# Performance work log

Hardware: AMD Instinct MI355X
Metric: run time of the kernel (lower is better)

## Reference

```python
import jax, jax.numpy as jnp
import numpy as np

DIM = 32
B, H, W = 4, 256, 256


def conv1x1(x, w, b):
    # x: [B,C,H,W], w: [O,C], b: [O]
    return jnp.einsum('bchw,oc->bohw', x, w) + b[None, :, None, None]


def conv3x3(x, w, b):
    # x: [B,C,H,W], w: [O,C,3,3]
    out = jax.lax.conv_general_dilated(
        x, w, window_strides=(1, 1), padding='SAME',
        dimension_numbers=('NCHW', 'OIHW', 'NCHW'))
    return out + b[None, :, None, None]


def fft2d(x):
    # fft2 over last two dims, then fftshift over ALL dims (torch default)
    f = jnp.fft.fftshift(jnp.fft.fft2(x, norm='ortho'))
    return jnp.concatenate([f.real, f.imag], axis=1)  # [B,2C,H,W]


def ifft2d(x):
    f = jnp.fft.ifftshift(x)  # over ALL dims (torch default)
    re, im = jnp.split(f, 2, axis=1)
    c = jax.lax.complex(re, im)
    return jnp.abs(jnp.fft.ifft2(c, norm='ortho'))  # [B,C,H,W]


def setup_inputs() -> dict:
    key = jax.random.key(0)
    ks = jax.random.split(key, 16)
    C = DIM
    s = 0.02  # small init keeps the global-HW dot products in a sane softmax range
    inp = {
        'x': jax.random.normal(ks[0], (B, C, H, W), jnp.float32),
        'y': jax.random.normal(ks[1], (B, C, H, W), jnp.float32),
        'wq': jax.random.normal(ks[2], (C, C), jnp.float32) * s,
        'bq': jnp.zeros((C,), jnp.float32),
        'wk': jax.random.normal(ks[3], (C, C), jnp.float32) * s,
        'bk': jnp.zeros((C,), jnp.float32),
        'wv': jax.random.normal(ks[4], (C, C), jnp.float32) * s,
        'bv': jnp.zeros((C,), jnp.float32),
        'wd': jax.random.normal(ks[5], (C, C), jnp.float32) * s,
        'bd': jnp.zeros((C,), jnp.float32),
        'wc': jax.random.normal(ks[6], (2 * C, 2 * C, 3, 3), jnp.float32) * s,
        'bc': jnp.zeros((2 * C,), jnp.float32),
        'wi': jax.random.normal(ks[7], (2 * C, 2 * C, 3, 3), jnp.float32) * s,
        'bi': jnp.zeros((2 * C,), jnp.float32),
    }
    return inp


def reference(x, y, wq, bq, wk, bk, wv, bv, wd, bd, wc, bc, wi, bi):
    b, c, h, w = x.shape
    xq = conv1x1(x, wq, bq).reshape(b, c, h * w)            # [B,C,HW]
    dft = conv3x3(fft2d(conv1x1(y, wd, bd)), wc, bc)        # [B,2C,H,W]
    yk, yv = jnp.split(dft, 2, axis=1)
    yk = conv1x1(yk, wk, bk).reshape(b, c, h * w)
    yv = conv1x1(yv, wv, bv).reshape(b, c, h * w)
    att = jnp.einsum('bcn,bdn->bcd', xq, yk)                # [B,C,C]
    att = jax.nn.softmax(att, axis=1)                       # softmax over dim=1 (as in torch)
    out = jnp.einsum('bcd,bdn->bcn', att, yv).reshape(b, c, h, w)
    out = out + ifft2d(conv3x3(jax.nn.relu(dft), wi, bi))
    return out
```

## Files before the change

### kernel.cpp

```cpp
#include <hip/hip_runtime.h>
#include <math.h>

#define HW_ (256*256)
#define CH 32
#define CH2 64
#define BATCH 4

typedef short bf16x8 __attribute__((ext_vector_type(8)));
typedef float f32x4 __attribute__((ext_vector_type(4)));

__device__ __forceinline__ unsigned short f2bf(float f) {
    union { float f; unsigned u; } v; v.f = f;
    unsigned r = v.u + 0x7fffu + ((v.u >> 16) & 1u);
    return (unsigned short)(r >> 16);
}
__device__ __forceinline__ float bf2f(unsigned h) {
    union { unsigned u; float f; } v; v.u = h << 16;
    return v.f;
}

__device__ __forceinline__ int ctof_slot(int s) {
    return s < 16 ? s + 16 : s < 32 ? s + 32 : s < 48 ? s - 32 : s - 16;
}

__device__ __forceinline__ float2 cmul(float2 a, float2 b) {
    return make_float2(a.x*b.x - a.y*b.y, a.x*b.y + a.y*b.x);
}

__device__ __forceinline__ uint4 relu_bf16x8(uint4 v) {
    unsigned* pv = (unsigned*)&v;
    #pragma unroll
    for (int q = 0; q < 4; ++q) {
        unsigned a = pv[q];
        unsigned lo = a & 0xffffu, hi = a >> 16;
        if (lo & 0x8000u) lo = 0;
        if (hi & 0x8000u) hi = 0;
        pv[q] = lo | (hi << 16);
    }
    return v;
}

__device__ __forceinline__ void build_tw4(float2* tw, float sign) {
    int tid = threadIdx.x;
    float ang = sign * 6.2831853071795864769f * (float)tid / 256.0f;
    float s, c; sincosf(ang, &s, &c);
    tw[tid] = make_float2(c, s);
}

template<int SGN>
__device__ __forceinline__ void fft16_reg(float2* x, const float2* tw) {
    float2 u[16];
    #pragma unroll
    for (int m0 = 0; m0 < 4; ++m0) {
        float2 x0 = x[m0], x1 = x[m0+4], x2 = x[m0+8], x3 = x[m0+12];
        float2 t0 = make_float2(x0.x+x2.x, x0.y+x2.y);
        float2 t1 = make_float2(x0.x-x2.x, x0.y-x2.y);
        float2 t2 = make_float2(x1.x+x3.x, x1.y+x3.y);
        float2 t3 = make_float2(x1.x-x3.x, x1.y-x3.y);
        float2 r  = make_float2(-SGN*t3.y, SGN*t3.x);
        u[m0*4+0] = make_float2(t0.x+t2.x, t0.y+t2.y);
        u[m0*4+1] = make_float2(t1.x+r.x,  t1.y+r.y);
        u[m0*4+2] = make_float2(t0.x-t2.x, t0.y-t2.y);
        u[m0*4+3] = make_float2(t1.x-r.x,  t1.y-r.y);
    }
    #pragma unroll
    for (int m0 = 1; m0 < 4; ++m0)
        #pragma unroll
        for (int a = 1; a < 4; ++a)
            u[m0*4+a] = cmul(u[m0*4+a], tw[(16*m0*a) & 255]);
    #pragma unroll
    for (int a = 0; a < 4; ++a) {
        float2 x0 = u[a], x1 = u[4+a], x2 = u[8+a], x3 = u[12+a];
        float2 t0 = make_float2(x0.x+x2.x, x0.y+x2.y);
        float2 t1 = make_float2(x0.x-x2.x, x0.y-x2.y);
        float2 t2 = make_float2(x1.x+x3.x, x1.y+x3.y);
        float2 t3 = make_float2(x1.x-x3.x, x1.y-x3.y);
        float2 r  = make_float2(-SGN*t3.y, SGN*t3.x);
        x[a]    = make_float2(t0.x+t2.x, t0.y+t2.y);
        x[a+4]  = make_float2(t1.x+r.x,  t1.y+r.y);
        x[a+8]  = make_float2(t0.x-t2.x, t0.y-t2.y);
        x[a+12] = make_float2(t1.x-r.x,  t1.y-r.y);
    }
}

template<int SGN>
__device__ __forceinline__ void fft_core16(float2* A, const float2* tw) {
    const int tid = threadIdx.x;
    const int l = tid >> 4;
    const int d = tid & 15;
    const int base = l*257;
    float2 x[16];
    #pragma unroll
    for (int n1 = 0; n1 < 16; ++n1) x[n1] = A[base + n1*16 + d];
    fft16_reg<SGN>(x, tw);
    #pragma unroll
    for (int k0 = 1; k0 < 16; ++k0) x[k0] = cmul(x[k0], tw[d*k0]);
    #pragma unroll
    for (int k0 = 0; k0 < 16; ++k0) A[base + k0*16 + ((d + k0) & 15)] = x[k0];
    __syncthreads();
    #pragma unroll
    for (int n0 = 0; n0 < 16; ++n0) x[n0] = A[base + d*16 + ((n0 + d) & 15)];
    fft16_reg<SGN>(x, tw);
    #pragma unroll
    for (int k1 = 0; k1 < 16; ++k1) A[base + d + k1*16] = x[k1];
    __syncthreads();
}

__global__ __launch_bounds__(256) void k_fft_fwd1(const unsigned short* __restrict__ yd, ushort2* __restrict__ CAt) {
    __shared__ float2 A[16*257];
    __shared__ float2 tw[256];
    build_tw4(tw, -1.0f);
    int blk = blockIdx.x;
    int bp = blk >> 4, h0 = (blk & 15) << 4;
    int b = bp >> 4, p = bp & 15;
    const float sc = 1.0f/16.0f;
    const unsigned short* s0 = yd + ((size_t)(b*CH + 2*p))*HW_ + (size_t)h0*256;
    const unsigned short* s1 = s0 + HW_;
    for (int idx = threadIdx.x; idx < 16*64; idx += 256) {
        int l = idx >> 6, w4 = (idx & 63) << 2;
        uint2 va = *(const uint2*)(s0 + l*256 + w4);
        uint2 vb = *(const uint2*)(s1 + l*256 + w4);
        A[l*257 + w4+0] = make_float2(bf2f(va.x & 0xffffu)*sc, bf2f(vb.x & 0xffffu)*sc);
        A[l*257 + w4+1] = make_float2(bf2f(va.x >> 16)*sc, bf2f(vb.x >> 16)*sc);
        A[l*257 + w4+2] = make_float2(bf2f(va.y & 0xffffu)*sc, bf2f(vb.y & 0xffffu)*sc);
        A[l*257 + w4+3] = make_float2(bf2f(va.y >> 16)*sc, bf2f(vb.y >> 16)*sc);
    }
    __syncthreads();
    fft_core16<-1>(A, tw);
    int t = threadIdx.x;
    unsigned short pk[32];
    #pragma unroll
    for (int l = 0; l < 16; ++l) {
        float2 v = A[l*257 + t];
        pk[2*l]   = f2bf(v.x);
        pk[2*l+1] = f2bf(v.y);
    }
    uint4* d4 = (uint4*)(CAt + (size_t)bp*HW_ + (size_t)t*256 + h0);
    const uint4* s4 = (const uint4*)pk;
    d4[0] = s4[0]; d4[1] = s4[1]; d4[2] = s4[2]; d4[3] = s4[3];
}

__global__ __launch_bounds__(256) void k_fft_fwd2(const ushort2* __restrict__ CAt, unsigned short* __restrict__ FSH) {
    __shared__ float2 A[16*257];
    __shared__ float2 tw[256];
    build_tw4(tw, -1.0f);
    int blk = blockIdx.x;
    int b = blk >> 8, ph = (blk >> 7) & 1, vu = blk & 127;
    bool sp = (vu == 0);
    int col0 = vu, col1 = sp ? 128 : (256 - vu);
    const float sc = 1.0f/16.0f;
    for (int idx = threadIdx.x; idx < 16*256; idx += 256) {
        int l = idx >> 8, h = idx & 255;
        int p = l >> 1, s = l & 1;
        int col = s ? col1 : col0;
        ushort2 v = CAt[((size_t)(b*16 + ph*8 + p)*256 + col)*256 + h];
        A[l*257 + h] = make_float2(bf2f(v.x)*sc, bf2f(v.y)*sc);
    }
    __syncthreads();
    fft_core16<-1>(A, tw);
    int t = threadIdx.x;
    int bt = (b + 2) & 3;
    int ht = (t + 128) & 255;
    int tn = (256 - t) & 255;
    #pragma unroll
    for (int s = 0; s < 2; ++s) {
        int v = s ? col1 : col0;
        int wt = (v + 128) & 255;
        unsigned short pk[32];
        #pragma unroll
        for (int p = 0; p < 8; ++p) {
            int lA = 2*p + s;
            int lB = sp ? lA : (2*p + 1 - s);
            float2 Za = A[lA*257 + t];
            float2 Zb = A[lB*257 + tn];
            float xr = (Za.x + Zb.x)*0.5f, xi = (Za.y - Zb.y)*0.5f;
            float dr = Za.x - Zb.x,        di = Za.y + Zb.y;
            float yr = di*0.5f,            yi = -dr*0.5f;
            pk[2*p]     = f2bf(xr);
            pk[2*p+1]   = f2bf(yr);
            pk[16+2*p]  = f2bf(xi);
            pk[17+2*p]  = f2bf(yi);
        }
        unsigned short* dst = FSH + ((((size_t)bt*256 + ht)*256 + wt)*64 + ph*32);
        uint4* d4 = (uint4*)dst;
        const uint4* s4 = (const uint4*)pk;
        d4[0] = s4[0]; d4[1] = s4[1]; d4[2] = s4[2]; d4[3] = s4[3];
    }
}

__global__ __launch_bounds__(256) void k_conv1x1w(const float* __restrict__ in, const float* __restrict__ w,
                                                  const float* __restrict__ bias, unsigned short* __restrict__ out,
                                                  const float* __restrict__ wc, const float* __restrict__ wi,
                                                  unsigned short* __restrict__ d1, unsigned short* __restrict__ d2) {
    __shared__ float ts[32*257];
    int blk = blockIdx.x;
    int tid = threadIdx.x;
    if (blk >= 1024) {
        int i = (blk - 1024)*256 + tid;
        int half = i >= 36864;
        int j = i - half*36864;
        int tap = j >> 12, rem = j & 4095, oc = rem >> 6, s = rem & 63;
        if (half) {
            d2[j] = f2bf(wi[((size_t)(oc*64 + s))*9 + tap]);
        } else {
            int ic = ctof_slot(s);
            d1[j] = f2bf(wc[((size_t)(oc*64 + ic))*9 + tap]);
        }
        return;
    }
    int b = blk >> 8, h = blk & 255;
    const float* src = in + (size_t)b*CH*HW_ + (size_t)h*256;
    for (int idx = tid; idx < 32*256; idx += 256) {
        int c = idx >> 8, ww = idx & 255;
        ts[c*257 + ww] = src[(size_t)c*HW_ + ww];
    }
    __syncthreads();
    float acc[32];
    #pragma unroll
    for (int o = 0; o < 32; ++o) acc[o] = bias[o];
    for (int c = 0; c < 32; ++c) {
        float v = ts[c*257 + tid];
        #pragma unroll
        for (int o = 0; o < 32; ++o) acc[o] += w[o*32 + c] * v;
    }
    unsigned short* dst = out + (size_t)b*CH*HW_ + (size_t)h*256 + tid;
    #pragma unroll
    for (int o = 0; o < 32; ++o) dst[(size_t)o*HW_] = f2bf(acc[o]);
}

template<int MODE>
__global__ __launch_bounds__(256) void k_conv3(const unsigned short* __restrict__ in_cl,
                                               const unsigned short* __restrict__ wpk,
                                               const float* __restrict__ bias,
                                               unsigned short* __restrict__ outp) {
    __shared__ __align__(16) char Xs[2112*16];
    __shared__ __align__(16) char Ws[1536*16];
    int tid = threadIdx.x;
    int blk = blockIdx.x;
    int wseg = blk & 3, hg = (blk >> 2) & 63, b = blk >> 8;
    int h0 = hg*4, w0 = wseg*64;

    const uint4* wsrc = (const uint4*)wpk;

    for (int gl = tid; gl < 2112; gl += 256) {
        int slot = gl / 528;
        int rem  = gl - slot*528;
        int col  = rem >> 3, hseg = rem & 7;
        int hh = h0 - 1 + slot;
        int wcol = w0 - 1 + col;
        uint4 v = make_uint4(0,0,0,0);
        if (hh >= 0 && hh < 256 && wcol >= 0 && wcol < 256) {
            v = *(const uint4*)(in_cl + (((size_t)(b*256 + hh)*256 + wcol)*64) + hseg*8);
            if (MODE == 1) v = relu_bf16x8(v);
        }
        *(uint4*)(Xs + ((gl << 4) ^ ((col & 7) << 4))) = v;
    }
    #pragma unroll
    for (int q = 0; q < 6; ++q) {
        int gw = tid + q*256;
        int oc = (gw >> 3) & 63;
        *(uint4*)(Ws + ((gw << 4) ^ ((oc & 7) << 4))) = wsrc[gw];
    }
    __syncthreads();

    int lane = tid & 63;
    int wv = tid >> 6;
    int l16 = lane & 15, lq = lane >> 4;

    f32x4 acc[4][4];
    #pragma unroll
    for (int i = 0; i < 4; ++i)
        #pragma unroll
        for (int j = 0; j < 4; ++j) acc[i][j] = (f32x4)0.0f;

    for (int dy = 0; dy < 3; ++dy) {
        uint4 xr0 = make_uint4(0,0,0,0), xr1 = make_uint4(0,0,0,0), xr2 = make_uint4(0,0,0,0);
        uint4 wr[6];
        if (dy < 2) {
            int hh = h0 + dy + 3;
            bool hv = hh < 256;
            {
                int gl = tid;
                int col = gl >> 3, hseg = gl & 7;
                int wcol = w0 - 1 + col;
                if (hv && wcol >= 0 && wcol < 256)
                    xr0 = *(const uint4*)(in_cl + (((size_t)(b*256 + hh)*256 + wcol)*64) + hseg*8);
            }
            {
                int gl = tid + 256;
                int col = gl >> 3, hseg = gl & 7;
                int wcol = w0 - 1 + col;
                if (hv && wcol >= 0 && wcol < 256)
                    xr1 = *(const uint4*)(in_cl + (((size_t)(b*256 + hh)*256 + wcol)*64) + hseg*8);
            }
            if (tid < 16) {
                int gl = tid + 512;
                int col = gl >> 3, hseg = gl & 7;
                int wcol = w0 - 1 + col;
                if (hv && wcol < 256)
                    xr2 = *(const uint4*)(in_cl + (((size_t)(b*256 + hh)*256 + wcol)*64) + hseg*8);
            }
            #pragma unroll
            for (int q = 0; q < 6; ++q)
                wr[q] = wsrc[(dy+1)*1536 + tid + q*256];
        }

        int slot = (wv + dy) & 3;
        #pragma unroll
        for (int dx = 0; dx < 3; ++dx) {
            #pragma unroll
            for (int kk = 0; kk < 2; ++kk) {
                int hseg = kk*4 + lq;
                bf16x8 xf[4], wf[4];
                #pragma unroll
                for (int j = 0; j < 4; ++j) {
                    int col = j*16 + l16 + dx;
                    int g = slot*528 + col*8 + hseg;
                    xf[j] = *(const bf16x8*)(Xs + ((g << 4) ^ ((col & 7) << 4)));
                }
                #pragma unroll
                for (int i = 0; i < 4; ++i) {
                    int oc = i*16 + l16;
                    int lw = dx*512 + oc*8 + hseg;
                    wf[i] = *(const bf16x8*)(Ws + ((lw << 4) ^ ((oc & 7) << 4)));
                    #pragma unroll
                    for (int j = 0; j < 4; ++j) {
                        if (MODE == 0)
                            acc[i][j] = __builtin_amdgcn_mfma_f32_16x16x32_bf16(wf[i], xf[j], acc[i][j], 0, 0, 0);
                        else
                            acc[i][j] = __builtin_amdgcn_mfma_f32_16x16x32_bf16(xf[j], wf[i], acc[i][j], 0, 0, 0);
                    }
                }
            }
        }

        if (dy < 2) {
            __syncthreads();
            int slotn = dy & 3;
            {
                int gl = tid;
                int col = gl >> 3;
                uint4 v = (MODE == 1) ? relu_bf16x8(xr0) : xr0;
                int g = slotn*528 + gl;
                *(uint4*)(Xs + ((g << 4) ^ ((col & 7) << 4))) = v;
            }
            {
                int gl = tid + 256;
                int col = gl >> 3;
                uint4 v = (MODE == 1) ? relu_bf16x8(xr1) : xr1;
                int g = slotn*528 + gl;
                *(uint4*)(Xs + ((g << 4) ^ ((col & 7) << 4))) = v;
            }
            if (tid < 16) {
                int gl = tid + 512;
                int col = gl >> 3;
                uint4 v = (MODE == 1) ? relu_bf16x8(xr2) : xr2;
                int g = slotn*528 + gl;
                *(uint4*)(Xs + ((g << 4) ^ ((col & 7) << 4))) = v;
            }
            #pragma unroll
            for (int q = 0; q < 6; ++q) {
                int gw = tid + q*256;
                int oc = (gw >> 3) & 63;
                *(uint4*)(Ws + ((gw << 4) ^ ((oc & 7) << 4))) = wr[q];
            }
            __syncthreads();
        }
    }

    int h = h0 + wv;
    if (MODE == 0) {
        #pragma unroll
        for (int j = 0; j < 4; ++j) {
            int px = w0 + j*16 + l16;
            unsigned short* orow = outp + (((size_t)b*256 + h)*256 + px)*64;
            #pragma unroll
            for (int i = 0; i < 4; ++i) {
                int oc0 = i*16 + lq*4;
                float4 bv = *(const float4*)(bias + oc0);
                unsigned short c0 = f2bf(acc[i][j][0] + bv.x);
                unsigned short c1 = f2bf(acc[i][j][1] + bv.y);
                unsigned short c2 = f2bf(acc[i][j][2] + bv.z);
                unsigned short c3 = f2bf(acc[i][j][3] + bv.w);
                uint2 u;
                u.x = (unsigned)c0 | ((unsigned)c1 << 16);
                u.y = (unsigned)c2 | ((unsigned)c3 << 16);
                *(uint2*)(orow + oc0) = u;
            }
        }
    } else {
        #pragma unroll
        for (int i = 0; i < 4; ++i) {
            int oc = i*16 + l16;
            float bv = bias[oc];
            unsigned short* oplane = outp + ((size_t)b*64 + oc)*HW_ + (size_t)h*256;
            #pragma unroll
            for (int j = 0; j < 4; ++j) {
                int px0 = w0 + j*16 + lq*4;
                unsigned short c0 = f2bf(acc[i][j][0] + bv);
                unsigned short c1 = f2bf(acc[i][j][1] + bv);
                unsigned short c2 = f2bf(acc[i][j][2] + bv);
                unsigned short c3 = f2bf(acc[i][j][3] + bv);
                uint2 u;
                u.x = (unsigned)c0 | ((unsigned)c1 << 16);
                u.y = (unsigned)c2 | ((unsigned)c3 << 16);
                *(uint2*)(oplane + px0) = u;
            }
        }
    }
}

__global__ __launch_bounds__(256) void k_gram(const float* __restrict__ x, const unsigned short* __restrict__ dcl,
                                              float* __restrict__ Mpart, float* __restrict__ Sxp, float* __restrict__ Sdp) {
    __shared__ __align__(16) float xs[32*132];
    __shared__ __align__(16) unsigned short dst_[32*136];
    __shared__ float mred[1024];
    __shared__ float sxred[32];
    __shared__ float sdred[32];
    int blk = blockIdx.x;
    int b = blk >> 7, chunk = blk & 127;
    int tid = threadIdx.x, lane = tid & 63, wv = tid >> 6;
    int l16 = lane & 15, lq = lane >> 4;
    for (int idx = tid; idx < 1024; idx += 256) mred[idx] = 0.0f;
    if (tid < 32) { sxred[tid] = 0.0f; sdred[tid] = 0.0f; }

    const float* xb = x + (size_t)b*CH*HW_;
    const unsigned short* db = dcl + (size_t)b*HW_*64;

    f32x4 acc[2][2];
    #pragma unroll
    for (int i = 0; i < 2; ++i)
        #pragma unroll
        for (int j = 0; j < 2; ++j) acc[i][j] = (f32x4)0.0f;
    float sx0 = 0, sx1 = 0, sd0 = 0, sd1 = 0;

    for (int q4 = 0; q4 < 4; ++q4) {
        int px0 = chunk*512 + q4*128;
        __syncthreads();
        #pragma unroll
        for (int p = 0; p < 4; ++p) {
            int g = tid + p*256;
            int c = g >> 5, k4 = (g & 31) << 2;
            *(float4*)&xs[c*132 + k4] = *(const float4*)(xb + (size_t)c*HW_ + px0 + k4);
        }
        #pragma unroll
        for (int p = 0; p < 2; ++p) {
            int g = tid + p*256;
            int px = g >> 2, quad = g & 3;
            uint4 v = *(const uint4*)(db + (size_t)(px0 + px)*64 + quad*8);
            const unsigned short* pv = (const unsigned short*)&v;
            #pragma unroll
            for (int u = 0; u < 8; ++u) dst_[(quad*8 + u)*136 + px] = pv[u];
        }
        __syncthreads();
        #pragma unroll
        for (int ks = 0; ks < 4; ++ks) {
            int k0 = ks*32 + lq*8;
            float4 xa = *(const float4*)&xs[l16*132 + k0];
            float4 xc = *(const float4*)&xs[l16*132 + k0 + 4];
            float4 ya = *(const float4*)&xs[(16+l16)*132 + k0];
            float4 yc = *(const float4*)&xs[(16+l16)*132 + k0 + 4];
            bf16x8 a0, a1;
            const float* pxa = (const float*)&xa;
            const float* pxc = (const float*)&xc;
            const float* pya = (const float*)&ya;
            const float* pyc = (const float*)&yc;
            #pragma unroll
            for (int j = 0; j < 4; ++j) {
                a0[j]   = (short)f2bf(pxa[j]);  sx0 += pxa[j];
                a0[4+j] = (short)f2bf(pxc[j]);  sx0 += pxc[j];
                a1[j]   = (short)f2bf(pya[j]);  sx1 += pya[j];
                a1[4+j] = (short)f2bf(pyc[j]);  sx1 += pyc[j];
            }
            bf16x8 b0 = *(const bf16x8*)&dst_[l16*136 + k0];
            bf16x8 b1 = *(const bf16x8*)&dst_[(16+l16)*136 + k0];
            #pragma unroll
            for (int j = 0; j < 8; ++j) {
                sd0 += bf2f((unsigned short)b0[j]);
                sd1 += bf2f((unsigned short)b1[j]);
            }
            acc[0][0] = __builtin_amdgcn_mfma_f32_16x16x32_bf16(a0, b0, acc[0][0], 0, 0, 0);
            acc[0][1] = __builtin_amdgcn_mfma_f32_16x16x32_bf16(a0, b1, acc[0][1], 0, 0, 0);
            acc[1][0] = __builtin_amdgcn_mfma_f32_16x16x32_bf16(a1, b0, acc[1][0], 0, 0, 0);
            acc[1][1] = __builtin_amdgcn_mfma_f32_16x16x32_bf16(a1, b1, acc[1][1], 0, 0, 0);
        }
    }
    __syncthreads();

    #pragma unroll
    for (int fi = 0; fi < 2; ++fi)
        #pragma unroll
        for (int fj = 0; fj < 2; ++fj)
            #pragma unroll
            for (int r = 0; r < 4; ++r)
                atomicAdd(&mred[(fi*16 + lq*4 + r)*32 + fj*16 + l16], acc[fi][fj][r]);

    sx0 += __shfl_xor(sx0, 16); sx0 += __shfl_xor(sx0, 32);
    sx1 += __shfl_xor(sx1, 16); sx1 += __shfl_xor(sx1, 32);
    sd0 += __shfl_xor(sd0, 16); sd0 += __shfl_xor(sd0, 32);
    sd1 += __shfl_xor(sd1, 16); sd1 += __shfl_xor(sd1, 32);
    if (lane < 16) {
        atomicAdd(&sxred[l16], sx0);
        atomicAdd(&sxred[l16 + 16], sx1);
        atomicAdd(&sdred[l16], sd0);
        atomicAdd(&sdred[l16 + 16], sd1);
    }
    __syncthreads();

    float* mp = Mpart + ((size_t)(b*128 + chunk))*1024;
    for (int idx = tid; idx < 1024; idx += 256) mp[idx] = mred[idx];
    if (tid < 32) {
        Sxp[(b*128 + chunk)*32 + tid] = sxred[tid];
        Sdp[(b*128 + chunk)*32 + tid] = sdred[tid];
    }
}

__global__ __launch_bounds__(256) void k_att(const float* __restrict__ Mpart, const float* __restrict__ Sxp,
                                              const float* __restrict__ Sdp,
                                              const float* __restrict__ wq, const float* __restrict__ bq,
                                              const float* __restrict__ wk, const float* __restrict__ bk,
                                              const float* __restrict__ wv, const float* __restrict__ bv,
                                              float* __restrict__ att2, float* __restrict__ sout) {
    __shared__ float Mls[1024], T1[1024], attls[32*33];
    __shared__ float wqs[1024], wks[1024], wvs[1024];
    __shared__ float q1[32], k1[32], sxs[32], sds[32];
    int tid = threadIdx.x;
    int b = blockIdx.x;
    for (int idx = tid; idx < 1024; idx += 256) { wqs[idx] = wq[idx]; wks[idx] = wk[idx]; wvs[idx] = wv[idx]; }
    #pragma unroll
    for (int q = 0; q < 4; ++q) {
        int o = tid + q*256;
        float s = 0;
        for (int c = 0; c < 128; ++c) s += Mpart[((size_t)(b*128 + c))*1024 + o];
        Mls[o] = s;
    }
    if (tid < 32) { float s = 0; for (int c = 0; c < 128; ++c) s += Sxp[(b*128 + c)*32 + tid]; sxs[tid] = s; }
    else if (tid < 64) { int e = tid - 32; float s = 0; for (int c = 0; c < 128; ++c) s += Sdp[(b*128 + c)*32 + e]; sds[e] = s; }
    __syncthreads();
    if (tid < 32) { float s=0; for (int a=0;a<32;++a) s += wqs[tid*32+a]*sxs[a]; q1[tid]=s; }
    else if (tid < 64) { int d=tid-32; float s=0; for (int e=0;e<32;++e) s += wks[d*32+e]*sds[e]; k1[d]=s; }
    for (int idx = tid; idx < 1024; idx += 256) {
        int c = idx >> 5, e = idx & 31;
        float s = 0;
        for (int a=0;a<32;++a) s += wqs[c*32+a]*Mls[a*32+e];
        T1[idx] = s;
    }
    __syncthreads();
    for (int idx = tid; idx < 1024; idx += 256) {
        int c = idx >> 5, d = idx & 31;
        float s = 0;
        for (int e=0;e<32;++e) s += T1[c*32+e]*wks[d*32+e];
        s += bq[c]*k1[d] + bk[d]*q1[c] + 65536.0f*bq[c]*bk[d];
        attls[c*33+d] = s;
    }
    __syncthreads();
    if (tid < 32) {
        int d = tid;
        float mx = -1e30f;
        for (int c=0;c<32;++c) mx = fmaxf(mx, attls[c*33+d]);
        float sum = 0;
        for (int c=0;c<32;++c) { float e_ = expf(attls[c*33+d]-mx); attls[c*33+d]=e_; sum+=e_; }
        float inv = 1.0f/sum;
        for (int c=0;c<32;++c) attls[c*33+d] *= inv;
    }
    __syncthreads();
    for (int idx = tid; idx < 1024; idx += 256) {
        int c = idx >> 5, e = idx & 31;
        float s = 0;
        for (int d=0; d<32; ++d) s += attls[c*33+d]*wvs[d*32+e];
        att2[b*1024 + idx] = s;
    }
    if (tid < 32) {
        float s=0; for (int d=0;d<32;++d) s += attls[tid*33+d]*bv[d];
        sout[b*32+tid] = s;
    }
}

__global__ __launch_bounds__(256) void k_fft_inv1(const unsigned short* __restrict__ G, ushort2* __restrict__ Z1T) {
    __shared__ float2 A[16*257];
    __shared__ float2 tw[256];
    build_tw4(tw, 1.0f);
    int blk = blockIdx.x;
    int bc = blk >> 4, w0 = (blk & 15) << 4;
    int b = bc >> 5, c = bc & 31;
    int bs = (b + 2) & 3;
    const float sc = 1.0f/16.0f;
    const unsigned short* gre = G + ((size_t)(bs*CH2 + c + 32))*HW_;
    const unsigned short* gim = G + ((size_t)(bs*CH2 + c))*HW_;
    {
        int h = threadIdx.x;
        int hs = (h + 128) & 255;
        int wsb = (w0 + 128) & 255;
        const uint4* pr = (const uint4*)(gre + (size_t)hs*256 + wsb);
        const uint4* pi = (const uint4*)(gim + (size_t)hs*256 + wsb);
        uint4 r0 = pr[0], r1 = pr[1];
        uint4 i0 = pi[0], i1 = pi[1];
        unsigned short re[16], im[16];
        *(uint4*)&re[0] = r0; *(uint4*)&re[8] = r1;
        *(uint4*)&im[0] = i0; *(uint4*)&im[8] = i1;
        #pragma unroll
        for (int l = 0; l < 16; ++l)
            A[l*257 + h] = make_float2(bf2f(re[l])*sc, bf2f(im[l])*sc);
    }
    __syncthreads();
    fft_core16<1>(A, tw);
    ushort2* dst = Z1T + (size_t)bc*HW_;
    for (int idx = threadIdx.x; idx < 16*256; idx += 256) {
        int l = idx >> 8, h = idx & 255;
        float2 v = A[l*257 + h];
        dst[(size_t)(w0 + l)*256 + h] = make_ushort2(f2bf(v.x), f2bf(v.y));
    }
}

__global__ __launch_bounds__(256) void k_fft_inv2(const ushort2* __restrict__ Z1T, unsigned short* __restrict__ Mag) {
    __shared__ float2 A[16*257];
    __shared__ float2 tw[256];
    build_tw4(tw, 1.0f);
    int blk = blockIdx.x;
    int bc = blk >> 4, h0 = (blk & 15) << 4;
    const float sc = 1.0f/16.0f;
    {
        int w = threadIdx.x;
        const uint4* src = (const uint4*)(Z1T + (size_t)bc*HW_ + (size_t)w*256 + h0);
        uint4 t0 = src[0], t1 = src[1], t2 = src[2], t3 = src[3];
        ushort2 vv[16];
        *(uint4*)&vv[0]  = t0; *(uint4*)&vv[4]  = t1;
        *(uint4*)&vv[8]  = t2; *(uint4*)&vv[12] = t3;
        #pragma unroll
        for (int l = 0; l < 16; ++l)
            A[l*257 + w] = make_float2(bf2f(vv[l].x)*sc, bf2f(vv[l].y)*sc);
    }
    __syncthreads();
    fft_core16<1>(A, tw);
    unsigned short* dst = Mag + (size_t)bc*HW_ + (size_t)h0*256;
    for (int idx = threadIdx.x; idx < 16*256; idx += 256) {
        int l = idx >> 8, w = idx & 255;
        float2 v = A[l*257 + w];
        dst[l*256 + w] = f2bf(sqrtf(v.x*v.x + v.y*v.y));
    }
}

__global__ __launch_bounds__(256) void k_out(const unsigned short* __restrict__ dcl, const float* __restrict__ att2,
                                             const float* __restrict__ sv, const unsigned short* __restrict__ Mag,
                                             float* __restrict__ out) {
    __shared__ __align__(16) float A2ls[1024];
    __shared__ float svls[32];
    int blk = blockIdx.x; int b = blk >> 8, h = blk & 255;
    int tid = threadIdx.x;
    for (int idx = tid; idx < 1024; idx += 256) A2ls[idx] = att2[b*1024 + idx];
    if (tid < 32) svls[tid] = sv[b*32 + tid];
    __syncthreads();
    int px = tid;
    const uint4* dvp = (const uint4*)(dcl + ((((size_t)b*256 + h)*256 + px)*64 + 32));
    uint4 d0 = dvp[0], d1 = dvp[1];
    unsigned u[8] = {d0.x, d0.y, d0.z, d0.w, d1.x, d1.y, d1.z, d1.w};
    float dv[32];
    #pragma unroll
    for (int i = 0; i < 8; ++i) {
        dv[2*i]   = bf2f(u[i] & 0xffffu);
        dv[2*i+1] = bf2f(u[i] >> 16);
    }
    float accv[32];
    #pragma unroll
    for (int c = 0; c < 32; ++c) accv[c] = svls[c];
    #pragma unroll
    for (int q = 0; q < 8; ++q) {
        #pragma unroll
        for (int c = 0; c < 32; ++c) {
            float4 a4 = *(const float4*)&A2ls[c*32 + q*4];
            accv[c] += a4.x*dv[q*4] + a4.y*dv[q*4+1] + a4.z*dv[q*4+2] + a4.w*dv[q*4+3];
        }
    }
    const unsigned short* mb = Mag + (size_t)b*CH*HW_ + (size_t)h*256 + px;
    float* ob = out + (size_t)b*CH*HW_ + (size_t)h*256 + px;
    #pragma unroll
    for (int c = 0; c < 32; ++c) ob[(size_t)c*HW_] = accv[c] + bf2f(mb[(size_t)c*HW_]);
}

extern "C" void kernel_launch(void* const* d_in, const int* in_sizes, int n_in,
                              void* d_out, int out_size, void* d_ws, size_t ws_size,
                              hipStream_t stream) {
    const float* x  = (const float*)d_in[0];
    const float* y  = (const float*)d_in[1];
    const float* wq = (const float*)d_in[2];
    const float* bq = (const float*)d_in[3];
    const float* wk = (const float*)d_in[4];
    const float* bk = (const float*)d_in[5];
    const float* wv = (const float*)d_in[6];
    const float* bv = (const float*)d_in[7];
    const float* wd = (const float*)d_in[8];
    const float* bd = (const float*)d_in[9];
    const float* wc = (const float*)d_in[10];
    const float* bc = (const float*)d_in[11];
    const float* wi = (const float*)d_in[12];
    const float* bi = (const float*)d_in[13];
    float* out = (float*)d_out;

    char* ws = (char*)d_ws;
    size_t o = 0;
    unsigned short* R1   = (unsigned short*)(ws + o); o += (size_t)BATCH*CH*HW_*2;
    ushort2*        CAt  = (ushort2*)(ws + o);        o += (size_t)BATCH*CH*HW_*4;
    unsigned short* FSHc = (unsigned short*)(ws + o); o += (size_t)BATCH*CH2*HW_*2;
    unsigned short* DFTc = (unsigned short*)(ws + o); o += (size_t)BATCH*CH2*HW_*2;
    unsigned short* Gpl  = (unsigned short*)(ws + o); o += (size_t)BATCH*CH2*HW_*2;
    unsigned short* wpk1 = (unsigned short*)(ws + o); o += 9*64*64*2;
    unsigned short* wpk2 = (unsigned short*)(ws + o); o += 9*64*64*2;
    float*          Mpart= (float*)(ws + o);          o += (size_t)512*1024*4;
    float*          Sxp  = (float*)(ws + o);          o += 512*32*4;
    float*          Sdp  = (float*)(ws + o);          o += 512*32*4;
    float*          A2b  = (float*)(ws + o);          o += 4096*4;
    float*          Svb  = (float*)(ws + o);          o += 128*4;
    if (ws_size < o) return;

    ushort2*        Z1T = CAt;
    unsigned short* Mag = R1;

    k_conv1x1w<<<1312, 256, 0, stream>>>(y, wd, bd, R1, wc, wi, wpk1, wpk2);
    k_fft_fwd1<<<1024, 256, 0, stream>>>(R1, CAt);
    k_fft_fwd2<<<1024, 256, 0, stream>>>(CAt, FSHc);
    k_conv3<0><<<1024, 256, 0, stream>>>(FSHc, wpk1, bc, DFTc);
    k_conv3<1><<<1024, 256, 0, stream>>>(DFTc, wpk2, bi, Gpl);
    k_gram<<<512, 256, 0, stream>>>(x, DFTc, Mpart, Sxp, Sdp);
    k_att<<<4, 256, 0, stream>>>(Mpart, Sxp, Sdp, wq, bq, wk, bk, wv, bv, A2b, Svb);
    k_fft_inv1<<<2048, 256, 0, stream>>>(Gpl, Z1T);
    k_fft_inv2<<<2048, 256, 0, stream>>>(Z1T, Mag);
    k_out<<<1024, 256, 0, stream>>>(DFTc, A2b, Svb, Mag, out);
}
```

Baseline: 271.0 us.

## Pad conv3 inputs with zero border and read activations directly from global

Stores the FFT output and first conv output in a zero-padded 258x258 channel-last layout, with a new border-zeroing kernel, so the 3x3 conv no longer needs bounds checks. The conv kernel drops its LDS input tile and instead loads input pixels straight from global memory (relying on cache) while double-buffering weights in LDS. It also sets an occupancy hint and swizzles the block order for locality. This saves LDS staging and barriers, but risks more global or L2 traffic per MFMA and adds an extra launch.

```diff
diff --git a/kernel.cpp b/kernel.cpp
--- a/kernel.cpp
+++ b/kernel.cpp
@@ -5,6 +5,7 @@
 #define CH 32
 #define CH2 64
 #define BATCH 4
+#define PPL ((size_t)258*258*64)
 
 typedef short bf16x8 __attribute__((ext_vector_type(8)));
 typedef float f32x4 __attribute__((ext_vector_type(4)));
@@ -104,6 +105,23 @@
     #pragma unroll
     for (int k1 = 0; k1 < 16; ++k1) A[base + d + k1*16] = x[k1];
     __syncthreads();
+}
+
+__global__ __launch_bounds__(64) void k_border(unsigned short* __restrict__ FSH, unsigned short* __restrict__ DFT) {
+    int blk = blockIdx.x;
+    int buf = blk / 1032;
+    int r = blk - buf*1032;
+    int b = r / 258;
+    int h = r - b*258;
+    unsigned short* base = (buf ? DFT : FSH) + (size_t)b*PPL + (size_t)h*258*64;
+    uint4 z = make_uint4(0,0,0,0);
+    if (h == 0 || h == 257) {
+        uint4* p = (uint4*)base;
+        for (int i = threadIdx.x; i < 2064; i += 64) p[i] = z;
+    } else {
+        if (threadIdx.x < 8) ((uint4*)base)[threadIdx.x] = z;
+        else if (threadIdx.x < 16) ((uint4*)(base + (size_t)257*64))[threadIdx.x - 8] = z;
+    }
 }
 
 __global__ __launch_bounds__(256) void k_fft_fwd1(const unsigned short* __restrict__ yd, ushort2* __restrict__ CAt) {
@@ -181,7 +199,7 @@
             pk[16+2*p]  = f2bf(xi);
             pk[17+2*p]  = f2bf(yi);
         }
-        unsigned short* dst = FSH + ((((size_t)bt*256 + ht)*256 + wt)*64 + ph*32);
+        unsigned short* dst = FSH + (size_t)bt*PPL + ((size_t)(ht + 1)*258 + (wt + 1))*64 + ph*32;
         uint4* d4 = (uint4*)dst;
         const uint4* s4 = (const uint4*)pk;
         d4[0] = s4[0]; d4[1] = s4[1]; d4[2] = s4[2]; d4[3] = s4[3];
@@ -229,32 +247,21 @@
 }
 
 template<int MODE>
-__global__ __launch_bounds__(256) void k_conv3(const unsigned short* __restrict__ in_cl,
-                                               const unsigned short* __restrict__ wpk,
-                                               const float* __restrict__ bias,
-                                               unsigned short* __restrict__ outp) {
-    __shared__ __align__(16) char Xs[2112*16];
-    __shared__ __align__(16) char Ws[1536*16];
+__global__ __launch_bounds__(256, 3) void k_conv3(const unsigned short* __restrict__ in_cl,
+                                                  const unsigned short* __restrict__ wpk,
+                                                  const float* __restrict__ bias,
+                                                  unsigned short* __restrict__ outp) {
+    __shared__ __align__(16) char Ws[49152];
     int tid = threadIdx.x;
     int blk = blockIdx.x;
-    int wseg = blk & 3, hg = (blk >> 2) & 63, b = blk >> 8;
+    int sb = ((blk & 7) << 7) | (blk >> 3);
+    int wseg = sb & 3, hg = (sb >> 2) & 63, b = sb >> 8;
     int h0 = hg*4, w0 = wseg*64;
+    int lane = tid & 63, wv = tid >> 6;
+    int l16 = lane & 15, lq = lane >> 4;
 
     const uint4* wsrc = (const uint4*)wpk;
 
-    for (int gl = tid; gl < 2112; gl += 256) {
-        int slot = gl / 528;
-        int rem  = gl - slot*528;
-        int col  = rem >> 3, hseg = rem & 7;
-        int hh = h0 - 1 + slot;
-        int wcol = w0 - 1 + col;
-        uint4 v = make_uint4(0,0,0,0);
-        if (hh >= 0 && hh < 256 && wcol >= 0 && wcol < 256) {
-            v = *(const uint4*)(in_cl + (((size_t)(b*256 + hh)*256 + wcol)*64) + hseg*8);
-            if (MODE == 1) v = relu_bf16x8(v);
-        }
-        *(uint4*)(Xs + ((gl << 4) ^ ((col & 7) << 4))) = v;
-    }
     #pragma unroll
     for (int q = 0; q < 6; ++q) {
         int gw = tid + q*256;
@@ -263,9 +270,7 @@
     }
     __syncthreads();
 
-    int lane = tid & 63;
-    int wv = tid >> 6;
-    int l16 = lane & 15, lq = lane >> 4;
+    const unsigned short* Pb = in_cl + (size_t)b*PPL;
 
     f32x4 acc[4][4];
     #pragma unroll
@@ -273,39 +278,19 @@
         #pragma unroll
         for (int j = 0; j < 4; ++j) acc[i][j] = (f32x4)0.0f;
 
+    #pragma unroll
     for (int dy = 0; dy < 3; ++dy) {
-        uint4 xr0 = make_uint4(0,0,0,0), xr1 = make_uint4(0,0,0,0), xr2 = make_uint4(0,0,0,0);
         uint4 wr[6];
         if (dy < 2) {
-            int hh = h0 + dy + 3;
-            bool hv = hh < 256;
-            {
-                int gl = tid;
-                int col = gl >> 3, hseg = gl & 7;
-                int wcol = w0 - 1 + col;
-                if (hv && wcol >= 0 && wcol < 256)
-                    xr0 = *(const uint4*)(in_cl + (((size_t)(b*256 + hh)*256 + wcol)*64) + hseg*8);
-            }
-            {
-                int gl = tid + 256;
-                int col = gl >> 3, hseg = gl & 7;
-                int wcol = w0 - 1 + col;
-                if (hv && wcol >= 0 && wcol < 256)
-                    xr1 = *(const uint4*)(in_cl + (((size_t)(b*256 + hh)*256 + wcol)*64) + hseg*8);
-            }
-            if (tid < 16) {
-                int gl = tid + 512;
-                int col = gl >> 3, hseg = gl & 7;
-                int wcol = w0 - 1 + col;
-                if (hv && wcol < 256)
-                    xr2 = *(const uint4*)(in_cl + (((size_t)(b*256 + hh)*256 + wcol)*64) + hseg*8);
-            }
             #pragma unroll
             for (int q = 0; q < 6; ++q)
                 wr[q] = wsrc[(dy+1)*1536 + tid + q*256];
         }
 
-        int slot = (wv + dy) & 3;
+        int hrow = h0 + wv + dy;
+        const unsigned short* Prow = Pb + (size_t)hrow*258*64;
+        const char* Wh = Ws + (dy & 1)*24576;
+
         #pragma unroll
         for (int dx = 0; dx < 3; ++dx) {
             #pragma unroll
@@ -314,15 +299,15 @@
                 bf16x8 xf[4], wf[4];
                 #pragma unroll
                 for (int j = 0; j < 4; ++j) {
-                    int col = j*16 + l16 + dx;
-                    int g = slot*528 + col*8 + hseg;
-                    xf[j] = *(const bf16x8*)(Xs + ((g << 4) ^ ((col & 7) << 4)));
+                    uint4 xu = *(const uint4*)(Prow + (size_t)(w0 + j*16 + l16 + dx)*64 + hseg*8);
+                    if (MODE == 1) xu = relu_bf16x8(xu);
+                    xf[j] = *(bf16x8*)&xu;
                 }
                 #pragma unroll
                 for (int i = 0; i < 4; ++i) {
                     int oc = i*16 + l16;
                     int lw = dx*512 + oc*8 + hseg;
-                    wf[i] = *(const bf16x8*)(Ws + ((lw << 4) ^ ((oc & 7) << 4)));
+                    wf[i] = *(const bf16x8*)(Wh + ((lw << 4) ^ ((oc & 7) << 4)));
                     #pragma unroll
                     for (int j = 0; j < 4; ++j) {
                         if (MODE == 0)
@@ -335,34 +320,12 @@
         }
 
         if (dy < 2) {
-            __syncthreads();
-            int slotn = dy & 3;
-            {
-                int gl = tid;
-                int col = gl >> 3;
-                uint4 v = (MODE == 1) ? relu_bf16x8(xr0) : xr0;
-                int g = slotn*528 + gl;
-                *(uint4*)(Xs + ((g << 4) ^ ((col & 7) << 4))) = v;
-            }
-            {
-                int gl = tid + 256;
-                int col = gl >> 3;
-                uint4 v = (MODE == 1) ? relu_bf16x8(xr1) : xr1;
-                int g = slotn*528 + gl;
-                *(uint4*)(Xs + ((g << 4) ^ ((col & 7) << 4))) = v;
-            }
-            if (tid < 16) {
-                int gl = tid + 512;
-                int col = gl >> 3;
-                uint4 v = (MODE == 1) ? relu_bf16x8(xr2) : xr2;
-                int g = slotn*528 + gl;
-                *(uint4*)(Xs + ((g << 4) ^ ((col & 7) << 4))) = v;
-            }
+            char* Wn = Ws + ((dy + 1) & 1)*24576;
             #pragma unroll
             for (int q = 0; q < 6; ++q) {
                 int gw = tid + q*256;
                 int oc = (gw >> 3) & 63;
-                *(uint4*)(Ws + ((gw << 4) ^ ((oc & 7) << 4))) = wr[q];
+                *(uint4*)(Wn + ((gw << 4) ^ ((oc & 7) << 4))) = wr[q];
             }
             __syncthreads();
         }
@@ -373,7 +336,7 @@
         #pragma unroll
         for (int j = 0; j < 4; ++j) {
             int px = w0 + j*16 + l16;
-            unsigned short* orow = outp + (((size_t)b*256 + h)*256 + px)*64;
+            unsigned short* orow = outp + (size_t)b*PPL + ((size_t)(h + 1)*258 + (px + 1))*64;
             #pragma unroll
             for (int i = 0; i < 4; ++i) {
                 int oc0 = i*16 + lq*4;
@@ -393,7 +356,7 @@
         for (int i = 0; i < 4; ++i) {
             int oc = i*16 + l16;
             float bv = bias[oc];
-            unsigned short* oplane = outp + ((size_t)b*64 + oc)*HW_ + (size_t)h*256;
+            unsigned short* oplane = outp + ((size_t)(b*64 + oc))*HW_ + (size_t)h*256;
             #pragma unroll
             for (int j = 0; j < 4; ++j) {
                 int px0 = w0 + j*16 + lq*4;
@@ -425,7 +388,6 @@
     if (tid < 32) { sxred[tid] = 0.0f; sdred[tid] = 0.0f; }
 
     const float* xb = x + (size_t)b*CH*HW_;
-    const unsigned short* db = dcl + (size_t)b*HW_*64;
 
     f32x4 acc[2][2];
     #pragma unroll
@@ -436,6 +398,8 @@
 
     for (int q4 = 0; q4 < 4; ++q4) {
         int px0 = chunk*512 + q4*128;
+        int hrow = px0 >> 8, wc0 = px0 & 255;
+        const unsigned short* drow = dcl + (size_t)b*PPL + ((size_t)(hrow + 1)*258 + (wc0 + 1))*64;
         __syncthreads();
         #pragma unroll
         for (int p = 0; p < 4; ++p) {
@@ -447,7 +411,7 @@
         for (int p = 0; p < 2; ++p) {
             int g = tid + p*256;
             int px = g >> 2, quad = g & 3;
-            uint4 v = *(const uint4*)(db + (size_t)(px0 + px)*64 + quad*8);
+            uint4 v = *(const uint4*)(drow + (size_t)px*64 + quad*8);
             const unsigned short* pv = (const unsigned short*)&v;
             #pragma unroll
             for (int u = 0; u < 8; ++u) dst_[(quad*8 + u)*136 + px] = pv[u];
@@ -651,7 +615,7 @@
     if (tid < 32) svls[tid] = sv[b*32 + tid];
     __syncthreads();
     int px = tid;
-    const uint4* dvp = (const uint4*)(dcl + ((((size_t)b*256 + h)*256 + px)*64 + 32));
+    const uint4* dvp = (const uint4*)(dcl + (size_t)b*PPL + ((size_t)(h + 1)*258 + (px + 1))*64 + 32);
     uint4 d0 = dvp[0], d1 = dvp[1];
     unsigned u[8] = {d0.x, d0.y, d0.z, d0.w, d1.x, d1.y, d1.z, d1.w};
     float dv[32];
@@ -700,8 +664,8 @@
     size_t o = 0;
     unsigned short* R1   = (unsigned short*)(ws + o); o += (size_t)BATCH*CH*HW_*2;
     ushort2*        CAt  = (ushort2*)(ws + o);        o += (size_t)BATCH*CH*HW_*4;
-    unsigned short* FSHc = (unsigned short*)(ws + o); o += (size_t)BATCH*CH2*HW_*2;
-    unsigned short* DFTc = (unsigned short*)(ws + o); o += (size_t)BATCH*CH2*HW_*2;
+    unsigned short* FSHc = (unsigned short*)(ws + o); o += (size_t)BATCH*PPL*2;
+    unsigned short* DFTc = (unsigned short*)(ws + o); o += (size_t)BATCH*PPL*2;
     unsigned short* Gpl  = (unsigned short*)(ws + o); o += (size_t)BATCH*CH2*HW_*2;
     unsigned short* wpk1 = (unsigned short*)(ws + o); o += 9*64*64*2;
     unsigned short* wpk2 = (unsigned short*)(ws + o); o += 9*64*64*2;
@@ -715,6 +679,7 @@
     ushort2*        Z1T = CAt;
     unsigned short* Mag = R1;
 
+    k_border<<<2064, 64, 0, stream>>>(FSHc, DFTc);
     k_conv1x1w<<<1312, 256, 0, stream>>>(y, wd, bd, R1, wc, wi, wpk1, wpk2);
     k_fft_fwd1<<<1024, 256, 0, stream>>>(R1, CAt);
     k_fft_fwd2<<<1024, 256, 0, stream>>>(CAt, FSHc);
```

After: 302.8 us. +11.8%, slower.
